# Performance work log

Measured on AMD Instinct MI355X. Metric: run time of the kernel, lower is better.

Reference implementation:

```python
import jax, jax.numpy as jnp
import numpy as np

B = 1024          # batch
H = 512           # hidden_dim
T = 256           # seq_len
CD = 2            # coord_dim
LAT = 64 + 64 + 128  # total latent dim


def setup_inputs() -> dict:
    key = jax.random.key(0)
    ks = jax.random.split(key, 20)
    s = 0.05  # weight init scale
    rn = lambda k, shp: (jax.random.normal(k, shp, dtype=jnp.float32) * s)
    return {
        "z_primitive": jax.random.normal(ks[0], (B, 64), dtype=jnp.float32),
        "z_skill": jax.random.normal(ks[1], (B, 64), dtype=jnp.float32),
        "z_style": jax.random.normal(ks[2], (B, 128), dtype=jnp.float32),
        "W_proj": rn(ks[3], (2 * H, LAT)),
        "b_proj": jnp.zeros((2 * H,), jnp.float32),
        "Wih1": rn(ks[4], (4 * H, CD)),
        "Whh1": rn(ks[5], (4 * H, H)),
        "bih1": jnp.zeros((4 * H,), jnp.float32),
        "bhh1": jnp.zeros((4 * H,), jnp.float32),
        "Wih2": rn(ks[6], (4 * H, H)),
        "Whh2": rn(ks[7], (4 * H, H)),
        "bih2": jnp.zeros((4 * H,), jnp.float32),
        "bhh2": jnp.zeros((4 * H,), jnp.float32),
        "Wo1": rn(ks[8], (H // 2, H)),
        "bo1": jnp.zeros((H // 2,), jnp.float32),
        "Wo2": rn(ks[9], (CD, H // 2)),
        "bo2": jnp.zeros((CD,), jnp.float32),
    }


def _lstm_cell(x, h, c, Wih, Whh, bih, bhh):
    # PyTorch gate order: i, f, g, o
    gates = x @ Wih.T + h @ Whh.T + (bih + bhh)
    i, f, g, o = jnp.split(gates, 4, axis=1)
    c_new = jax.nn.sigmoid(f) * c + jax.nn.sigmoid(i) * jnp.tanh(g)
    h_new = jax.nn.sigmoid(o) * jnp.tanh(c_new)
    return h_new, c_new


def reference(z_primitive, z_skill, z_style, W_proj, b_proj,
              Wih1, Whh1, bih1, bhh1, Wih2, Whh2, bih2, bhh2,
              Wo1, bo1, Wo2, bo2):
    z = jnp.concatenate([z_primitive, z_skill, z_style], axis=1)  # [B, LAT]
    init = z @ W_proj.T + b_proj                                  # [B, 2H]
    h0 = init[:, :H]
    c0 = init[:, H:]
    x0 = jnp.zeros((z.shape[0], CD), init.dtype)

    def step(carry, _):
        x, h1, c1, h2, c2 = carry
        h1, c1 = _lstm_cell(x, h1, c1, Wih1, Whh1, bih1, bhh1)
        h2, c2 = _lstm_cell(h1, h2, c2, Wih2, Whh2, bih2, bhh2)
        # output MLP (Dropout inactive in eval)
        y = jax.nn.relu(h2 @ Wo1.T + bo1) @ Wo2.T + bo2  # [B, CD]
        return (y, h1, c1, h2, c2), y

    # h0/c0 repeated across both LSTM layers (repeat(2,1,1) in torch)
    _, ys = jax.lax.scan(step, (x0, h0, c0, h0, c0), None, length=T)
    return jnp.transpose(ys, (1, 0, 2))  # [B, T, CD]
```

## Files before the change

kernel.cpp:

```cpp
#include <hip/hip_runtime.h>
#include <math.h>

#define NB 1024
#define NH 512
#define NT 256
#define NCD 2

typedef unsigned short u16;
typedef __bf16 bf16x8 __attribute__((ext_vector_type(8)));
typedef float  f32x4  __attribute__((ext_vector_type(4)));

#define MFMA_BF16 __builtin_amdgcn_mfma_f32_16x16x32_bf16

__device__ __forceinline__ float sigf(float x) { return 1.0f / (1.0f + expf(-x)); }
__device__ __forceinline__ u16 f2b(float f) {
    union { float f; unsigned i; } v; v.f = f;
    unsigned r = v.i + 0x7fffu + ((v.i >> 16) & 1u);
    return (u16)(r >> 16);
}

__device__ __forceinline__ void async_cp16(const void* gptr, void* lptr) {
    __builtin_amdgcn_global_load_lds(
        (const __attribute__((address_space(1))) unsigned int*)gptr,
        (__attribute__((address_space(3))) unsigned int*)lptr,
        16, 0, 0);
}

__device__ __forceinline__ float aloadf(const float* p) {
    return __hip_atomic_load((float*)p, __ATOMIC_RELAXED, __HIP_MEMORY_SCOPE_AGENT);
}

__global__ __launch_bounds__(256) void convert3(
    const float* __restrict__ a, const float* __restrict__ b,
    const float* __restrict__ c,
    u16* __restrict__ oa, u16* __restrict__ ob, u16* __restrict__ oc)
{
    const int i = blockIdx.x * 256 + threadIdx.x;
    oa[i] = f2b(a[i]); ob[i] = f2b(b[i]); oc[i] = f2b(c[i]);
}

__global__ __launch_bounds__(256) void convw1(
    const float* __restrict__ a, u16* __restrict__ o)
{
    const int i = blockIdx.x * 256 + threadIdx.x;
    o[i] = f2b(a[i]);
}

__global__ __launch_bounds__(256) void bsum_k(
    const float* __restrict__ bi1, const float* __restrict__ bh1,
    const float* __restrict__ bi2, const float* __restrict__ bh2,
    float* __restrict__ o1, float* __restrict__ o2)
{
    const int i = blockIdx.x * 256 + threadIdx.x;
    o1[i] = bi1[i] + bh1[i];
    o2[i] = bi2[i] + bh2[i];
}

__global__ __launch_bounds__(512) void zero_bar(unsigned* __restrict__ b)
{
    b[threadIdx.x] = 0u;
}

__global__ __launch_bounds__(512) void zero_out(float* __restrict__ o)
{
    o[blockIdx.x * 512 + threadIdx.x] = 0.f;
}

__global__ __launch_bounds__(256) void init_kernel(
    const float* __restrict__ zp, const float* __restrict__ zs,
    const float* __restrict__ zst, const float* __restrict__ Wp,
    const float* __restrict__ bp,
    u16* __restrict__ h1, float* __restrict__ c1,
    u16* __restrict__ h2, float* __restrict__ c2)
{
    __shared__ float z[4][256];
    const int tid = threadIdx.x;
    const int b0  = blockIdx.x * 4;
    for (int i = tid; i < 4 * 256; i += 256) {
        const int bb = i >> 8, k = i & 255;
        float v;
        if (k < 64)       v = zp [(b0 + bb) * 64  + k];
        else if (k < 128) v = zs [(b0 + bb) * 64  + (k - 64)];
        else              v = zst[(b0 + bb) * 128 + (k - 128)];
        z[bb][k] = v;
    }
    __syncthreads();
    for (int rt = 0; rt < 4; ++rt) {
        const int r = rt * 256 + tid;
        const float bias = bp[r];
        float a0 = bias, a1 = bias, a2 = bias, a3 = bias;
        for (int k = 0; k < 256; ++k) {
            const float w = Wp[r * 256 + k];
            a0 += z[0][k] * w; a1 += z[1][k] * w;
            a2 += z[2][k] * w; a3 += z[3][k] * w;
        }
        const float acc[4] = {a0, a1, a2, a3};
        for (int bb = 0; bb < 4; ++bb) {
            const int b = b0 + bb;
            if (r < NH) {
                h1[b * NH + r] = f2b(acc[bb]);
                h2[b * NH + r] = f2b(acc[bb]);
            } else {
                c1[b * NH + r - NH] = acc[bb];
                c2[b * NH + r - NH] = acc[bb];
            }
        }
    }
}

__global__ __launch_bounds__(512, 4) void fused_out_lstm1(
    const u16* __restrict__ h2prev,
    const u16* __restrict__ A0,
    const u16* __restrict__ W0,
    const float* __restrict__ bsum,
    const float* __restrict__ Wx,
    const u16* __restrict__ W1b,
    const float* __restrict__ bo1, const float* __restrict__ Wo2,
    const float* __restrict__ bo2, float* __restrict__ outp,
    float* __restrict__ c, u16* __restrict__ hnext,
    unsigned* __restrict__ bar,
    const int t, const int do_lstm)
{
    __shared__ __align__(16) char smem[61440];
    float* eg  = (float*)smem;

    const int tid  = threadIdx.x;
    const int lane = tid & 63;
    const int wv   = tid >> 6;
    const int g    = wv & 3;
    const int mh   = wv >> 2;
    const int l15  = lane & 15;
    const int q    = lane >> 4;
    const int bx   = blockIdx.x;
    const int ut   = (bx & 7) * 2 + ((bx >> 3) & 1);
    const int grp  = bx >> 4;
    const int b0   = grp * 32;
    const int u0   = ut * 32;
    const bool has_prev = (h2prev != 0);

    int goffW0, goffW1, goffA = 0, goffWS = 0;
    {
        const int c0 = (wv * 2) * 64 + lane;
        const int w0r = c0 >> 3;
        goffW0 = ((w0r >> 5) * NH + u0 + (w0r & 31)) * NH + (((c0 & 7) ^ (w0r & 7)) * 8);
        const int c1i = (wv * 2 + 1) * 64 + lane;
        const int w1r = c1i >> 3;
        goffW1 = ((w1r >> 5) * NH + u0 + (w1r & 31)) * NH + (((c1i & 7) ^ (w1r & 7)) * 8);
        if (wv < 4) {
            const int ca = wv * 64 + lane;
            const int ar = ca >> 3;
            goffA = (b0 + ar) * NH + (((ca & 7) ^ (ar & 7)) * 8);
        }
        if (wv == 4 || wv == 5) {
            const int cs = (wv - 4) * 64 + lane;
            const int rl = cs >> 3;
            goffWS = (ut * 16 + rl) * NH + (((cs & 7) ^ (rl & 7)) * 8);
        }
    }

    auto issueL = [&](int m, int s) {
        const int k0 = (m & 7) * 64;
        char* base = smem + s * 20480;
        async_cp16((const void*)(W0 + goffW0 + k0),
                   (void*)(base + 4096 + (wv * 2) * 1024));
        async_cp16((const void*)(W0 + goffW1 + k0),
                   (void*)(base + 4096 + (wv * 2 + 1) * 1024));
        if (wv < 4)
            async_cp16((const void*)(A0 + goffA + k0),
                       (void*)(base + wv * 1024));
    };
    auto issue_pa = [&](int k, int pb) {
        const int k0 = k * 64;
        char* base = smem + 40960 + pb * 6144;
        if (wv < 4)
            async_cp16((const void*)(h2prev + goffA + k0),
                       (void*)(base + (wv << 10)));
        if (wv == 4 || wv == 5)
            async_cp16((const void*)(W1b + goffWS + k0),
                       (void*)(base + 4096 + ((wv - 4) << 10)));
    };

    const int u_e  = tid & 31;
    const int bq_e = tid >> 5;
    const int ug_e = u0 + u_e;
    float bs[4], wx0[4], wx1[4], cpre[2];
#pragma unroll
    for (int g4 = 0; g4 < 4; ++g4) bs[g4] = bsum[g4 * NH + ug_e];
#pragma unroll
    for (int g4 = 0; g4 < 4; ++g4) {
        wx0[g4] = Wx[(g4 * NH + ug_e) * 2 + 0];
        wx1[g4] = Wx[(g4 * NH + ug_e) * 2 + 1];
    }
    cpre[0] = c[(size_t)(b0 + bq_e * 2 + 0) * NH + ug_e];
    cpre[1] = c[(size_t)(b0 + bq_e * 2 + 1) * NH + ug_e];

    f32x4 acc_o[2], acc[2];
    acc_o[0] = (f32x4){0.f, 0.f, 0.f, 0.f};
    acc_o[1] = (f32x4){0.f, 0.f, 0.f, 0.f};
    acc[0]   = (f32x4){0.f, 0.f, 0.f, 0.f};
    acc[1]   = (f32x4){0.f, 0.f, 0.f, 0.f};

    if (do_lstm) issueL(0, 0);
    if (has_prev) { issue_pa(0, 0); issue_pa(1, 1); }

    for (int k = 0; k < 8; ++k) {
        if (has_prev && k < 7 && wv < 6)
            asm volatile("s_waitcnt vmcnt(1)" ::: "memory");
        else
            asm volatile("s_waitcnt vmcnt(0)" ::: "memory");
        __builtin_amdgcn_s_barrier();
        if (do_lstm && k + 1 < 8) issueL(k + 1, (k + 1) & 1);
        if (has_prev && k + 2 < 8) {
            int pb = k + 2; while (pb >= 3) pb -= 3;
            issue_pa(k + 2, pb);
        }
        if (has_prev) {
            int cp = k; while (cp >= 3) cp -= 3;
            const char* pbase = smem + 40960 + cp * 6144;
#pragma unroll
            for (int kh = 0; kh < 2; ++kh) {
                const int j = (kh * 4 + q) ^ (l15 & 7);
                const bf16x8 bfr = *(const bf16x8*)(pbase + 4096 + l15 * 128 + j * 16);
#pragma unroll
                for (int mi = 0; mi < 2; ++mi) {
                    const bf16x8 av = *(const bf16x8*)(pbase + (mi * 16 + l15) * 128 + j * 16);
                    acc_o[mi] = MFMA_BF16(av, bfr, acc_o[mi], 0, 0, 0);
                }
            }
        }
        if (do_lstm) {
            const char* bA = smem + (k & 1) * 20480;
            const char* bW = bA + 4096;
#pragma unroll
            for (int khi = 0; khi < 2; ++khi) {
                bf16x8 bfr[2];
#pragma unroll
                for (int ni = 0; ni < 2; ++ni) {
                    const int wrow = g * 32 + ni * 16 + l15;
                    const int j = (khi * 4 + q) ^ (wrow & 7);
                    bfr[ni] = *(const bf16x8*)(bW + wrow * 128 + j * 16);
                }
                const int row = mh * 16 + l15;
                const int j = (khi * 4 + q) ^ (row & 7);
                const bf16x8 av = *(const bf16x8*)(bA + row * 128 + j * 16);
                acc[0] = MFMA_BF16(av, bfr[0], acc[0], 0, 0, 0);
                acc[1] = MFMA_BF16(av, bfr[1], acc[1], 0, 0, 0);
            }
        }
    }

    if (has_prev) {
        const int ng = ut * 16 + l15;
        const float bo1n = bo1[ng];
        const float w20  = Wo2[ng];
        const float w21  = Wo2[256 + ng];
        float pa[2][4], pb[2][4];
#pragma unroll
        for (int mi = 0; mi < 2; ++mi)
#pragma unroll
            for (int r = 0; r < 4; ++r) {
                const float s = fmaxf(acc_o[mi][r] + bo1n, 0.f);
                pa[mi][r] = s * w20;
                pb[mi][r] = s * w21;
            }
#pragma unroll
        for (int off = 1; off < 16; off <<= 1)
#pragma unroll
            for (int mi = 0; mi < 2; ++mi)
#pragma unroll
                for (int r = 0; r < 4; ++r) {
                    pa[mi][r] += __shfl_xor(pa[mi][r], off, 64);
                    pb[mi][r] += __shfl_xor(pb[mi][r], off, 64);
                }
        if (wv == 0 && l15 == 0) {
            const float b20 = (ut == 0) ? bo2[0] : 0.f;
            const float b21 = (ut == 0) ? bo2[1] : 0.f;
#pragma unroll
            for (int mi = 0; mi < 2; ++mi)
#pragma unroll
                for (int r = 0; r < 4; ++r) {
                    const int m = mi * 16 + q * 4 + r;
                    float* dst = outp + (size_t)(b0 + m) * (NT * NCD) + (t - 1) * NCD;
                    atomicAdd(dst + 0, pa[mi][r] + b20);
                    atomicAdd(dst + 1, pb[mi][r] + b21);
                }
        }
    }
    if (!do_lstm) return;

    __syncthreads();
#pragma unroll
    for (int ni = 0; ni < 2; ++ni)
#pragma unroll
        for (int r = 0; r < 4; ++r)
            eg[(g * 32 + mh * 16 + q * 4 + r) * 33 + ni * 16 + l15] = acc[ni][r];
    __syncthreads();

    float r_x[4] = {0.f, 0.f, 0.f, 0.f};
    if (has_prev) {
        unsigned* mybar = bar + grp * 16;
        const unsigned target = 16u * (unsigned)t;
        if (tid == 0) {
            __hip_atomic_fetch_add(mybar, 1u, __ATOMIC_RELAXED, __HIP_MEMORY_SCOPE_AGENT);
            int guard = 0;
            while (__hip_atomic_load(mybar, __ATOMIC_RELAXED, __HIP_MEMORY_SCOPE_AGENT)
                       < target && ++guard < (1 << 20)) {
                __builtin_amdgcn_s_sleep(1);
            }
        }
        __syncthreads();
#pragma unroll
        for (int jj = 0; jj < 2; ++jj) {
            const float* src = outp + (size_t)(b0 + bq_e * 2 + jj) * (NT * NCD)
                               + (t - 1) * NCD;
            r_x[jj * 2 + 0] = aloadf(src + 0);
            r_x[jj * 2 + 1] = aloadf(src + 1);
        }
    }

#pragma unroll
    for (int jj = 0; jj < 2; ++jj) {
        const int bl = bq_e * 2 + jj;
        const int b  = b0 + bl;
        float gv[4];
#pragma unroll
        for (int g4 = 0; g4 < 4; ++g4) gv[g4] = eg[(g4 * 32 + bl) * 33 + u_e] + bs[g4];
        const float x0 = r_x[jj * 2 + 0];
        const float x1 = r_x[jj * 2 + 1];
#pragma unroll
        for (int g4 = 0; g4 < 4; ++g4) gv[g4] += x0 * wx0[g4] + x1 * wx1[g4];
        const float iv = sigf(gv[0]);
        const float fv = sigf(gv[1]);
        const float gg = tanhf(gv[2]);
        const float ov = sigf(gv[3]);
        const size_t idx = (size_t)b * NH + ug_e;
        const float cn = fv * cpre[jj] + iv * gg;
        c[idx] = cn;
        hnext[idx] = f2b(ov * tanhf(cn));
    }
}

__global__ __launch_bounds__(512, 4) void lstm_mfma32(
    const u16* __restrict__ A0, const u16* __restrict__ W0,
    const u16* __restrict__ A1, const u16* __restrict__ W1,
    const float* __restrict__ bsum,
    float* __restrict__ c, u16* __restrict__ hnext,
    const int npass)
{
    __shared__ __align__(16) char smem[61440];
    float* eg = (float*)smem;

    const int tid  = threadIdx.x;
    const int lane = tid & 63;
    const int wv   = tid >> 6;
    const int g    = wv & 3;
    const int mh   = wv >> 2;
    const int l15  = lane & 15;
    const int q    = lane >> 4;
    const int bx   = blockIdx.x;
    const int ut   = (bx & 7) * 2 + ((bx >> 3) & 1);
    const int grp  = bx >> 4;
    const int b0   = grp * 32;
    const int u0   = ut * 32;

    int goffW0, goffW1, goffA = 0;
    {
        const int c0 = (wv * 2) * 64 + lane;
        const int w0r = c0 >> 3;
        goffW0 = ((w0r >> 5) * NH + u0 + (w0r & 31)) * NH + (((c0 & 7) ^ (w0r & 7)) * 8);
        const int c1i = (wv * 2 + 1) * 64 + lane;
        const int w1r = c1i >> 3;
        goffW1 = ((w1r >> 5) * NH + u0 + (w1r & 31)) * NH + (((c1i & 7) ^ (w1r & 7)) * 8);
        if (wv < 4) {
            const int ca = wv * 64 + lane;
            const int ar = ca >> 3;
            goffA = (b0 + ar) * NH + (((ca & 7) ^ (ar & 7)) * 8);
        }
    }

    const int u_e  = tid & 31;
    const int bq_e = tid >> 5;
    const int ug_e = u0 + u_e;
    float bs[4], cpre[2];
#pragma unroll
    for (int g4 = 0; g4 < 4; ++g4) bs[g4] = bsum[g4 * NH + ug_e];
    cpre[0] = c[(size_t)(b0 + bq_e * 2 + 0) * NH + ug_e];
    cpre[1] = c[(size_t)(b0 + bq_e * 2 + 1) * NH + ug_e];

    f32x4 acc[2];
    acc[0] = (f32x4){0.f, 0.f, 0.f, 0.f};
    acc[1] = (f32x4){0.f, 0.f, 0.f, 0.f};

    const int M = npass * 8;

    auto issue = [&](int m, int bi) {
        const u16* __restrict__ Ap = (m < 8) ? A0 : A1;
        const u16* __restrict__ Wp = (m < 8) ? W0 : W1;
        const int k0 = (m & 7) * 64;
        char* base = smem + bi * 20480;
        async_cp16((const void*)(Wp + goffW0 + k0),
                   (void*)(base + 4096 + (wv * 2) * 1024));
        async_cp16((const void*)(Wp + goffW1 + k0),
                   (void*)(base + 4096 + (wv * 2 + 1) * 1024));
        if (wv < 4)
            async_cp16((const void*)(Ap + goffA + k0),
                       (void*)(base + wv * 1024));
    };

    issue(0, 0);
    if (M > 1) issue(1, 1);
    int ci = 0;
    for (int m = 0; m < M; ++m) {
        if (m + 1 < M) {
            if (wv < 4) asm volatile("s_waitcnt vmcnt(3)" ::: "memory");
            else        asm volatile("s_waitcnt vmcnt(2)" ::: "memory");
        } else {
            asm volatile("s_waitcnt vmcnt(0)" ::: "memory");
        }
        __builtin_amdgcn_s_barrier();
        if (m + 2 < M) {
            int bi = ci + 2; if (bi >= 3) bi -= 3;
            issue(m + 2, bi);
        }
        const char* bA = smem + ci * 20480;
        const char* bW = bA + 4096;
#pragma unroll
        for (int khi = 0; khi < 2; ++khi) {
            bf16x8 bfr[2];
#pragma unroll
            for (int ni = 0; ni < 2; ++ni) {
                const int wrow = g * 32 + ni * 16 + l15;
                const int j = (khi * 4 + q) ^ (wrow & 7);
                bfr[ni] = *(const bf16x8*)(bW + wrow * 128 + j * 16);
            }
            const int row = mh * 16 + l15;
            const int j = (khi * 4 + q) ^ (row & 7);
            const bf16x8 av = *(const bf16x8*)(bA + row * 128 + j * 16);
            acc[0] = MFMA_BF16(av, bfr[0], acc[0], 0, 0, 0);
            acc[1] = MFMA_BF16(av, bfr[1], acc[1], 0, 0, 0);
        }
        ++ci; if (ci == 3) ci = 0;
    }

    __syncthreads();
#pragma unroll
    for (int ni = 0; ni < 2; ++ni)
#pragma unroll
        for (int r = 0; r < 4; ++r)
            eg[(g * 32 + mh * 16 + q * 4 + r) * 33 + ni * 16 + l15] = acc[ni][r];
    __syncthreads();

#pragma unroll
    for (int jj = 0; jj < 2; ++jj) {
        const int bl = bq_e * 2 + jj;
        const int b  = b0 + bl;
        float gv[4];
#pragma unroll
        for (int g4 = 0; g4 < 4; ++g4) gv[g4] = eg[(g4 * 32 + bl) * 33 + u_e] + bs[g4];
        const float iv = sigf(gv[0]);
        const float fv = sigf(gv[1]);
        const float gg = tanhf(gv[2]);
        const float ov = sigf(gv[3]);
        const size_t idx = (size_t)b * NH + ug_e;
        const float cn = fv * cpre[jj] + iv * gg;
        c[idx] = cn;
        hnext[idx] = f2b(ov * tanhf(cn));
    }
}

extern "C" void kernel_launch(void* const* d_in, const int* in_sizes, int n_in,
                              void* d_out, int out_size, void* d_ws, size_t ws_size,
                              hipStream_t stream)
{
    const float* zp   = (const float*)d_in[0];
    const float* zsk  = (const float*)d_in[1];
    const float* zst  = (const float*)d_in[2];
    const float* Wp   = (const float*)d_in[3];
    const float* bp   = (const float*)d_in[4];
    const float* Wih1 = (const float*)d_in[5];
    const float* Whh1 = (const float*)d_in[6];
    const float* bih1 = (const float*)d_in[7];
    const float* bhh1 = (const float*)d_in[8];
    const float* Wih2 = (const float*)d_in[9];
    const float* Whh2 = (const float*)d_in[10];
    const float* bih2 = (const float*)d_in[11];
    const float* bhh2 = (const float*)d_in[12];
    const float* Wo1  = (const float*)d_in[13];
    const float* bo1  = (const float*)d_in[14];
    const float* Wo2  = (const float*)d_in[15];
    const float* bo2  = (const float*)d_in[16];

    const size_t BH = (size_t)NB * NH;
    u16*   h1a   = (u16*)d_ws;
    u16*   h1b   = h1a + BH;
    u16*   h2a   = h1b + BH;
    u16*   h2b   = h2a + BH;
    float* c1    = (float*)(h2b + BH);
    float* c2    = c1 + BH;
    float* bs1   = c2 + BH;
    float* bs2   = bs1 + 2048;
    u16*   Wo1b  = (u16*)(bs2 + 2048);
    u16*   Whh1b = Wo1b + 131072;
    u16*   Wih2b = Whh1b + 1048576;
    u16*   Whh2b = Wih2b + 1048576;
    unsigned* bar = (unsigned*)(Whh2b + 1048576);

    convert3<<<(2048 * 512) / 256, 256, 0, stream>>>(Whh1, Wih2, Whh2, Whh1b, Wih2b, Whh2b);
    convw1<<<(256 * 512) / 256, 256, 0, stream>>>(Wo1, Wo1b);
    bsum_k<<<2048 / 256, 256, 0, stream>>>(bih1, bhh1, bih2, bhh2, bs1, bs2);
    init_kernel<<<NB / 4, 256, 0, stream>>>(zp, zsk, zst, Wp, bp, h1a, c1, h2a, c2);
    zero_bar<<<1, 512, 0, stream>>>(bar);
    zero_out<<<(NB * NT * NCD) / 512, 512, 0, stream>>>((float*)d_out);

    u16* h1c = h1a; u16* h1n = h1b;
    u16* h2c = h2a; u16* h2n = h2b;
    float* outp = (float*)d_out;
    for (int t = 0; t < NT; ++t) {
        fused_out_lstm1<<<512, 512, 0, stream>>>(
            (t == 0) ? (const u16*)0 : h2c, h1c, Whh1b, bs1, Wih1,
            Wo1b, bo1, Wo2, bo2, outp, c1, h1n, bar, t, 1);
        lstm_mfma32<<<512, 512, 0, stream>>>(h1n, Wih2b, h2c, Whh2b,
                                             bs2, c2, h2n, 2);
        u16* tmp = h1c; h1c = h1n; h1n = tmp;
        tmp = h2c; h2c = h2n; h2n = tmp;
    }
    fused_out_lstm1<<<512, 512, 0, stream>>>(
        h2c, h1c, Whh1b, bs1, Wih1,
        Wo1b, bo1, Wo2, bo2, outp, c1, h1n, bar, NT, 0);
}
```

Measured before the change: 6.824 ms.

## Interleave both layer-2 GEMM operands in a double-buffered dual-stream K loop

The layer-2 LSTM kernel used to walk the Wih2·h1 and Whh2·h2 products one after the other through a 16-step, triple-buffered pipeline. It now runs both products together over 8 K-steps. Each step double-buffers loads for both operand pairs into 80KB of dynamic shared memory and keeps two independent accumulator sets, which are summed before the gate math. This halves the barrier count and gives more independent MFMA work per step. The costs are a larger LDS footprint, which may cut blocks per CU, and a full vmcnt(0) wait each step in place of partial waits.

Measured after the change: 7.059 ms. +3.4%, slower.

```diff
diff --git a/kernel.cpp b/kernel.cpp
--- a/kernel.cpp
+++ b/kernel.cpp
@@ -340,14 +340,13 @@
     }
 }
 
-__global__ __launch_bounds__(512, 4) void lstm_mfma32(
+__global__ __launch_bounds__(512, 4) void lstm2_dual(
     const u16* __restrict__ A0, const u16* __restrict__ W0,
     const u16* __restrict__ A1, const u16* __restrict__ W1,
     const float* __restrict__ bsum,
-    float* __restrict__ c, u16* __restrict__ hnext,
-    const int npass)
-{
-    __shared__ __align__(16) char smem[61440];
+    float* __restrict__ c, u16* __restrict__ hnext)
+{
+    extern __shared__ char smem[];
     float* eg = (float*)smem;
 
     const int tid  = threadIdx.x;
@@ -387,17 +386,9 @@
     cpre[0] = c[(size_t)(b0 + bq_e * 2 + 0) * NH + ug_e];
     cpre[1] = c[(size_t)(b0 + bq_e * 2 + 1) * NH + ug_e];
 
-    f32x4 acc[2];
-    acc[0] = (f32x4){0.f, 0.f, 0.f, 0.f};
-    acc[1] = (f32x4){0.f, 0.f, 0.f, 0.f};
-
-    const int M = npass * 8;
-
-    auto issue = [&](int m, int bi) {
-        const u16* __restrict__ Ap = (m < 8) ? A0 : A1;
-        const u16* __restrict__ Wp = (m < 8) ? W0 : W1;
+    auto issueX = [&](const u16* __restrict__ Ap, const u16* __restrict__ Wp,
+                      int m, char* base) {
         const int k0 = (m & 7) * 64;
-        char* base = smem + bi * 20480;
         async_cp16((const void*)(Wp + goffW0 + k0),
                    (void*)(base + 4096 + (wv * 2) * 1024));
         async_cp16((const void*)(Wp + goffW1 + k0),
@@ -406,23 +397,7 @@
             async_cp16((const void*)(Ap + goffA + k0),
                        (void*)(base + wv * 1024));
     };
-
-    issue(0, 0);
-    if (M > 1) issue(1, 1);
-    int ci = 0;
-    for (int m = 0; m < M; ++m) {
-        if (m + 1 < M) {
-            if (wv < 4) asm volatile("s_waitcnt vmcnt(3)" ::: "memory");
-            else        asm volatile("s_waitcnt vmcnt(2)" ::: "memory");
-        } else {
-            asm volatile("s_waitcnt vmcnt(0)" ::: "memory");
-        }
-        __builtin_amdgcn_s_barrier();
-        if (m + 2 < M) {
-            int bi = ci + 2; if (bi >= 3) bi -= 3;
-            issue(m + 2, bi);
-        }
-        const char* bA = smem + ci * 20480;
+    auto mstep = [&](const char* bA, f32x4* a2) {
         const char* bW = bA + 4096;
 #pragma unroll
         for (int khi = 0; khi < 2; ++khi) {
@@ -436,10 +411,31 @@
             const int row = mh * 16 + l15;
             const int j = (khi * 4 + q) ^ (row & 7);
             const bf16x8 av = *(const bf16x8*)(bA + row * 128 + j * 16);
-            acc[0] = MFMA_BF16(av, bfr[0], acc[0], 0, 0, 0);
-            acc[1] = MFMA_BF16(av, bfr[1], acc[1], 0, 0, 0);
-        }
-        ++ci; if (ci == 3) ci = 0;
+            a2[0] = MFMA_BF16(av, bfr[0], a2[0], 0, 0, 0);
+            a2[1] = MFMA_BF16(av, bfr[1], a2[1], 0, 0, 0);
+        }
+    };
+
+    f32x4 accP[2], accQ[2];
+    accP[0] = (f32x4){0.f, 0.f, 0.f, 0.f};
+    accP[1] = (f32x4){0.f, 0.f, 0.f, 0.f};
+    accQ[0] = (f32x4){0.f, 0.f, 0.f, 0.f};
+    accQ[1] = (f32x4){0.f, 0.f, 0.f, 0.f};
+
+    issueX(A0, W0, 0, smem + 0);
+    issueX(A1, W1, 0, smem + 40960);
+
+    for (int k = 0; k < 8; ++k) {
+        asm volatile("s_waitcnt vmcnt(0)" ::: "memory");
+        __builtin_amdgcn_s_barrier();
+        if (k + 1 < 8) {
+            char* pB = smem + ((k + 1) & 1) * 20480;
+            char* qB = smem + 40960 + ((k + 1) & 1) * 20480;
+            issueX(A0, W0, k + 1, pB);
+            issueX(A1, W1, k + 1, qB);
+        }
+        mstep(smem + (k & 1) * 20480, accP);
+        mstep(smem + 40960 + (k & 1) * 20480, accQ);
     }
 
     __syncthreads();
@@ -447,7 +443,8 @@
     for (int ni = 0; ni < 2; ++ni)
 #pragma unroll
         for (int r = 0; r < 4; ++r)
-            eg[(g * 32 + mh * 16 + q * 4 + r) * 33 + ni * 16 + l15] = acc[ni][r];
+            eg[(g * 32 + mh * 16 + q * 4 + r) * 33 + ni * 16 + l15] =
+                accP[ni][r] + accQ[ni][r];
     __syncthreads();
 
 #pragma unroll
@@ -505,6 +502,14 @@
     u16*   Whh2b = Wih2b + 1048576;
     unsigned* bar = (unsigned*)(Whh2b + 1048576);
 
+    static bool attr_done = false;
+    if (!attr_done) {
+        (void)hipFuncSetAttribute((const void*)lstm2_dual,
+                                  hipFuncAttributeMaxDynamicSharedMemorySize,
+                                  81920);
+        attr_done = true;
+    }
+
     convert3<<<(2048 * 512) / 256, 256, 0, stream>>>(Whh1, Wih2, Whh2, Whh1b, Wih2b, Whh2b);
     convw1<<<(256 * 512) / 256, 256, 0, stream>>>(Wo1, Wo1b);
     bsum_k<<<2048 / 256, 256, 0, stream>>>(bih1, bhh1, bih2, bhh2, bs1, bs2);
@@ -519,8 +524,8 @@
         fused_out_lstm1<<<512, 512, 0, stream>>>(
             (t == 0) ? (const u16*)0 : h2c, h1c, Whh1b, bs1, Wih1,
             Wo1b, bo1, Wo2, bo2, outp, c1, h1n, bar, t, 1);
-        lstm_mfma32<<<512, 512, 0, stream>>>(h1n, Wih2b, h2c, Whh2b,
-                                             bs2, c2, h2n, 2);
+        lstm2_dual<<<512, 512, 81920, stream>>>(h1n, Wih2b, h2c, Whh2b,
+                                                bs2, c2, h2n);
         u16* tmp = h1c; h1c = h1n; h1n = tmp;
         tmp = h2c; h2c = h2n; h2n = tmp;
     }
```
